# Kernel tuning notes

Hardware: AMD Instinct MI355X
Metric: run time of the kernel (lower is better)

The kernel has to match this reference:

```python
import jax, jax.numpy as jnp
import numpy as np

GAMMA = 0.96875  # RetNet decay, 1 - 2**-5


def setup_inputs() -> dict:
    key = jax.random.key(0)
    kq, kk, kv = jax.random.split(key, 3)
    B, T, D = 8, 4096, 64
    q = jax.random.normal(kq, (B, T, D), dtype=jnp.float32)
    k = jax.random.normal(kk, (B, T, D), dtype=jnp.float32)
    v = jax.random.normal(kv, (B, T, D), dtype=jnp.float32)
    return {"q": q, "k": k, "v": v}


def reference(q, k, v):
    # Parallel retention: out = (QK^T * D_gamma / sqrt(d)) V,
    # D_gamma[i,j] = gamma^(i-j) for i>=j else 0.
    B, T, D = q.shape
    dtype = q.dtype
    idx = jnp.arange(T)
    diff = idx[:, None] - idx[None, :]           # [T,T]
    gamma = jnp.asarray(GAMMA, dtype)
    decay = jnp.where(
        diff >= 0,
        gamma ** jnp.maximum(diff, 0).astype(dtype),
        jnp.zeros((), dtype),
    )                                            # [T,T] causal decay mask
    qk = jnp.einsum('btd,bsd->bts', q, k)        # [B,T,T]
    scale = jnp.asarray(np.sqrt(D), dtype)
    attn = qk * decay[None, :, :] / scale        # [B,T,T]
    out = jnp.einsum('bts,bsd->btd', attn, v)    # [B,T,D]
    return out
```

## Files before the change

kernel.cpp:

```cpp
#include <hip/hip_runtime.h>


using bf16x8 = __attribute__((ext_vector_type(8))) short;
using bf16x4 = __attribute__((ext_vector_type(4))) short;
using f32x4  = __attribute__((ext_vector_type(4))) float;

#define T_SEQ  4096
#define DHEAD  64
#define BM     64
#define BN     64
#define LDSS   72
#define NBACK  3

__device__ __forceinline__ short f2bf(float f) {
  union { float fv; unsigned u; } un; un.fv = f;
  unsigned r = un.u + 0x7FFFu + ((un.u >> 16) & 1u);
  return (short)(r >> 16);
}

__global__ __launch_bounds__(256, 3)
void retention_fwd(const float* __restrict__ qg,
                   const float* __restrict__ kg,
                   const float* __restrict__ vg,
                   float* __restrict__ outg) {
  constexpr float L2G   = -0.04580368961312478f;
  constexpr float GAMMA = 0.96875f;
  constexpr float GI16  = 1.6619242819629204f;
  constexpr float SCALE = 0.125f;

  __shared__ short lds_q [BM * LDSS];
  __shared__ short lds_k [BN * LDSS];
  __shared__ short lds_vt[DHEAD * LDSS];
  __shared__ short lds_p [4 * 16 * LDSS];

  const int tid  = threadIdx.x;
  const int lane = tid & 63;
  const int w    = tid >> 6;
  const int qt   = blockIdx.x & 63;
  const int b    = blockIdx.x >> 6;
  const int iq0  = qt * BM;
  const long base = (long)b * T_SEQ * DHEAD;

  const int ntiles = (qt < NBACK ? qt : NBACK) + 1;

  float4 kreg[4], vreg[4];
  const float4* kbase4 = reinterpret_cast<const float4*>(kg + base);
  const float4* vbase4 = reinterpret_cast<const float4*>(vg + base);

  auto load_kv = [&](int jk0) {
    const float4* ksrc = kbase4 + jk0 * (DHEAD / 4);
    const float4* vsrc = vbase4 + jk0 * (DHEAD / 4);
#pragma unroll
    for (int rep = 0; rep < 4; ++rep) {
      kreg[rep] = ksrc[tid + rep * 256];
      vreg[rep] = vsrc[tid + rep * 256];
    }
  };

  auto stage_kv = [&]() {
#pragma unroll
    for (int rep = 0; rep < 4; ++rep) {
      int idx = tid + rep * 256;
      int row = idx >> 4;
      int c4  = idx & 15;
      bf16x4 s4;
      s4[0] = f2bf(kreg[rep].x); s4[1] = f2bf(kreg[rep].y);
      s4[2] = f2bf(kreg[rep].z); s4[3] = f2bf(kreg[rep].w);
      *reinterpret_cast<bf16x4*>(&lds_k[row * LDSS + c4 * 4]) = s4;
      lds_vt[(c4 * 4 + 0) * LDSS + row] = f2bf(vreg[rep].x);
      lds_vt[(c4 * 4 + 1) * LDSS + row] = f2bf(vreg[rep].y);
      lds_vt[(c4 * 4 + 2) * LDSS + row] = f2bf(vreg[rep].z);
      lds_vt[(c4 * 4 + 3) * LDSS + row] = f2bf(vreg[rep].w);
    }
  };

  {
    const float4* qsrc = reinterpret_cast<const float4*>(qg + base + (long)iq0 * DHEAD);
    float4 qreg[4];
#pragma unroll
    for (int rep = 0; rep < 4; ++rep) qreg[rep] = qsrc[tid + rep * 256];
    load_kv(iq0);
#pragma unroll
    for (int rep = 0; rep < 4; ++rep) {
      int idx = tid + rep * 256;
      int row = idx >> 4;
      int c4  = idx & 15;
      bf16x4 s4;
      s4[0] = f2bf(qreg[rep].x); s4[1] = f2bf(qreg[rep].y);
      s4[2] = f2bf(qreg[rep].z); s4[3] = f2bf(qreg[rep].w);
      *reinterpret_cast<bf16x4*>(&lds_q[row * LDSS + c4 * 4]) = s4;
    }
    stage_kv();
  }
  __syncthreads();

  const int koff = (lane >> 4) * 8;
  const int l15  = lane & 15;
  bf16x8 qf0, qf1;
  {
    int row = w * 16 + l15;
    qf0 = *reinterpret_cast<const bf16x8*>(&lds_q[row * LDSS + koff]);
    qf1 = *reinterpret_cast<const bf16x8*>(&lds_q[row * LDSS + 32 + koff]);
  }

  f32x4 oacc[4];
#pragma unroll
  for (int dt = 0; dt < 4; ++dt) { oacc[dt][0]=0.f; oacc[dt][1]=0.f; oacc[dt][2]=0.f; oacc[dt][3]=0.f; }

  for (int t = 0; t < ntiles; ++t) {
    const int delta = t * BN;
    const bool pf = (t + 1 < ntiles);
    if (pf) load_kv(iq0 - (t + 1) * BN);

    bf16x8 kf[4][2], vf[4][2];
#pragma unroll
    for (int nt = 0; nt < 4; ++nt) {
      int frow = (nt * 16 + l15) * LDSS + koff;
      kf[nt][0] = *reinterpret_cast<const bf16x8*>(&lds_k[frow]);
      kf[nt][1] = *reinterpret_cast<const bf16x8*>(&lds_k[frow + 32]);
      vf[nt][0] = *reinterpret_cast<const bf16x8*>(&lds_vt[frow]);
      vf[nt][1] = *reinterpret_cast<const bf16x8*>(&lds_vt[frow + 32]);
    }
    asm volatile("s_waitcnt lgkmcnt(0)" ::: "memory");
    __syncthreads();

    const int mi = (lane >> 4) * 4;
    const int ebase0 = delta + w * 16 + mi - l15;
    float gq = exp2f((float)ebase0 * L2G) * SCALE;
#pragma unroll
    for (int nt = 0; nt < 4; ++nt) {
      f32x4 s; s[0]=0.f; s[1]=0.f; s[2]=0.f; s[3]=0.f;
      s = __builtin_amdgcn_mfma_f32_16x16x32_bf16(qf0, kf[nt][0], s, 0, 0, 0);
      s = __builtin_amdgcn_mfma_f32_16x16x32_bf16(qf1, kf[nt][1], s, 0, 0, 0);
      const int ebase = ebase0 - nt * 16;
      float g = gq;
#pragma unroll
      for (int r = 0; r < 4; ++r) {
        float sc = ((ebase + r) >= 0) ? g : 0.0f;
        lds_p[(w * 16 + mi + r) * LDSS + nt * 16 + l15] = f2bf(s[r] * sc);
        g *= GAMMA;
      }
      gq *= GI16;
    }
    asm volatile("s_waitcnt lgkmcnt(0)" ::: "memory");

    {
      int prow = (w * 16 + l15) * LDSS + koff;
      bf16x8 pf0 = *reinterpret_cast<const bf16x8*>(&lds_p[prow]);
      bf16x8 pf1 = *reinterpret_cast<const bf16x8*>(&lds_p[prow + 32]);
      __builtin_amdgcn_s_setprio(1);
#pragma unroll
      for (int dt = 0; dt < 4; ++dt) {
        oacc[dt] = __builtin_amdgcn_mfma_f32_16x16x32_bf16(pf0, vf[dt][0], oacc[dt], 0, 0, 0);
        oacc[dt] = __builtin_amdgcn_mfma_f32_16x16x32_bf16(pf1, vf[dt][1], oacc[dt], 0, 0, 0);
      }
      __builtin_amdgcn_s_setprio(0);
    }

    if (pf) stage_kv();
    __syncthreads();
  }

#pragma unroll
  for (int dt = 0; dt < 4; ++dt) {
#pragma unroll
    for (int r = 0; r < 4; ++r) {
      int i = iq0 + w * 16 + (lane >> 4) * 4 + r;
      int d = dt * 16 + l15;
      outg[base + (long)i * DHEAD + d] = oacc[dt][r];
    }
  }
}

extern "C" void kernel_launch(void* const* d_in, const int* in_sizes, int n_in,
                              void* d_out, int out_size, void* d_ws, size_t ws_size,
                              hipStream_t stream) {
  const float* q = (const float*)d_in[0];
  const float* k = (const float*)d_in[1];
  const float* v = (const float*)d_in[2];
  float* out = (float*)d_out;
  int total_rows = in_sizes[0] / DHEAD;
  int nblocks = total_rows / BM;
  retention_fwd<<<dim3(nblocks), dim3(256), 0, stream>>>(q, k, v, out);
}
```

Baseline: 84.61 us.

## Split key tiles across two wave groups per block and reduce partial outputs

Doubles the block to 512 threads. The two halves of four waves each process alternating key tiles for the same query tile, each using its own K/V LDS buffers, and their partial output accumulators are summed through LDS at the end. The aim is to halve the serial tile loop per block (at most 4 tiles become 2 rounds) and raise wave-level parallelism. The cost is a larger LDS footprint (~63KB), which likely limits how many blocks fit per CU, plus an extra reduction step and barriers. K/V fragments are now loaded from LDS inside the compute loop instead of being held in registers beforehand.

```diff
diff --git a/kernel.cpp b/kernel.cpp
--- a/kernel.cpp
+++ b/kernel.cpp
@@ -18,7 +18,7 @@
   return (short)(r >> 16);
 }
 
-__global__ __launch_bounds__(256, 3)
+__global__ __launch_bounds__(512, 4)
 void retention_fwd(const float* __restrict__ qg,
                    const float* __restrict__ kg,
                    const float* __restrict__ vg,
@@ -28,20 +28,29 @@
   constexpr float GI16  = 1.6619242819629204f;
   constexpr float SCALE = 0.125f;
 
-  __shared__ short lds_q [BM * LDSS];
-  __shared__ short lds_k [BN * LDSS];
-  __shared__ short lds_vt[DHEAD * LDSS];
-  __shared__ short lds_p [4 * 16 * LDSS];
+  __shared__ __align__(16) char smem[64512];
+  short* lds_q  = (short*)(smem);
+  short* lds_kb = (short*)(smem + 9216);
+  short* lds_vb = (short*)(smem + 27648);
+  short* lds_p  = (short*)(smem + 46080);
+  float* lds_red= (float*)(smem + 46080);
 
   const int tid  = threadIdx.x;
   const int lane = tid & 63;
   const int w    = tid >> 6;
+  const int mw   = w & 3;
+  const int hw   = w >> 2;
+  const int tid2 = tid & 255;
   const int qt   = blockIdx.x & 63;
   const int b    = blockIdx.x >> 6;
   const int iq0  = qt * BM;
   const long base = (long)b * T_SEQ * DHEAD;
 
-  const int ntiles = (qt < NBACK ? qt : NBACK) + 1;
+  const int ntiles  = (qt < NBACK ? qt : NBACK) + 1;
+  const int nrounds = (ntiles + 1) >> 1;
+
+  short* lds_k  = lds_kb + hw * (BN * LDSS);
+  short* lds_vt = lds_vb + hw * (BN * LDSS);
 
   float4 kreg[4], vreg[4];
   const float4* kbase4 = reinterpret_cast<const float4*>(kg + base);
@@ -52,15 +61,15 @@
     const float4* vsrc = vbase4 + jk0 * (DHEAD / 4);
 #pragma unroll
     for (int rep = 0; rep < 4; ++rep) {
-      kreg[rep] = ksrc[tid + rep * 256];
-      vreg[rep] = vsrc[tid + rep * 256];
+      kreg[rep] = ksrc[tid2 + rep * 256];
+      vreg[rep] = vsrc[tid2 + rep * 256];
     }
   };
 
   auto stage_kv = [&]() {
 #pragma unroll
     for (int rep = 0; rep < 4; ++rep) {
-      int idx = tid + rep * 256;
+      int idx = tid2 + rep * 256;
       int row = idx >> 4;
       int c4  = idx & 15;
       bf16x4 s4;
@@ -75,14 +84,16 @@
   };
 
   {
+    const int t0 = hw;
+    const bool v0 = (t0 < ntiles);
     const float4* qsrc = reinterpret_cast<const float4*>(qg + base + (long)iq0 * DHEAD);
-    float4 qreg[4];
-#pragma unroll
-    for (int rep = 0; rep < 4; ++rep) qreg[rep] = qsrc[tid + rep * 256];
-    load_kv(iq0);
-#pragma unroll
-    for (int rep = 0; rep < 4; ++rep) {
-      int idx = tid + rep * 256;
+    float4 qreg[2];
+#pragma unroll
+    for (int rep = 0; rep < 2; ++rep) qreg[rep] = qsrc[tid + rep * 512];
+    if (v0) load_kv(iq0 - t0 * BN);
+#pragma unroll
+    for (int rep = 0; rep < 2; ++rep) {
+      int idx = tid + rep * 512;
       int row = idx >> 4;
       int c4  = idx & 15;
       bf16x4 s4;
@@ -90,7 +101,7 @@
       s4[2] = f2bf(qreg[rep].z); s4[3] = f2bf(qreg[rep].w);
       *reinterpret_cast<bf16x4*>(&lds_q[row * LDSS + c4 * 4]) = s4;
     }
-    stage_kv();
+    if (v0) stage_kv();
   }
   __syncthreads();
 
@@ -98,7 +109,7 @@
   const int l15  = lane & 15;
   bf16x8 qf0, qf1;
   {
-    int row = w * 16 + l15;
+    int row = mw * 16 + l15;
     qf0 = *reinterpret_cast<const bf16x8*>(&lds_q[row * LDSS + koff]);
     qf1 = *reinterpret_cast<const bf16x8*>(&lds_q[row * LDSS + 32 + koff]);
   }
@@ -107,67 +118,85 @@
 #pragma unroll
   for (int dt = 0; dt < 4; ++dt) { oacc[dt][0]=0.f; oacc[dt][1]=0.f; oacc[dt][2]=0.f; oacc[dt][3]=0.f; }
 
-  for (int t = 0; t < ntiles; ++t) {
-    const int delta = t * BN;
-    const bool pf = (t + 1 < ntiles);
-    if (pf) load_kv(iq0 - (t + 1) * BN);
-
-    bf16x8 kf[4][2], vf[4][2];
-#pragma unroll
-    for (int nt = 0; nt < 4; ++nt) {
-      int frow = (nt * 16 + l15) * LDSS + koff;
-      kf[nt][0] = *reinterpret_cast<const bf16x8*>(&lds_k[frow]);
-      kf[nt][1] = *reinterpret_cast<const bf16x8*>(&lds_k[frow + 32]);
-      vf[nt][0] = *reinterpret_cast<const bf16x8*>(&lds_vt[frow]);
-      vf[nt][1] = *reinterpret_cast<const bf16x8*>(&lds_vt[frow + 32]);
-    }
-    asm volatile("s_waitcnt lgkmcnt(0)" ::: "memory");
-    __syncthreads();
-
-    const int mi = (lane >> 4) * 4;
-    const int ebase0 = delta + w * 16 + mi - l15;
-    float gq = exp2f((float)ebase0 * L2G) * SCALE;
-#pragma unroll
-    for (int nt = 0; nt < 4; ++nt) {
-      f32x4 s; s[0]=0.f; s[1]=0.f; s[2]=0.f; s[3]=0.f;
-      s = __builtin_amdgcn_mfma_f32_16x16x32_bf16(qf0, kf[nt][0], s, 0, 0, 0);
-      s = __builtin_amdgcn_mfma_f32_16x16x32_bf16(qf1, kf[nt][1], s, 0, 0, 0);
-      const int ebase = ebase0 - nt * 16;
-      float g = gq;
-#pragma unroll
-      for (int r = 0; r < 4; ++r) {
-        float sc = ((ebase + r) >= 0) ? g : 0.0f;
-        lds_p[(w * 16 + mi + r) * LDSS + nt * 16 + l15] = f2bf(s[r] * sc);
-        g *= GAMMA;
-      }
-      gq *= GI16;
-    }
-    asm volatile("s_waitcnt lgkmcnt(0)" ::: "memory");
-
-    {
+  for (int r = 0; r < nrounds; ++r) {
+    const int t     = 2 * r + hw;
+    const bool valid = (t < ntiles);
+    const int tn    = t + 2;
+    const bool pf   = (tn < ntiles);
+    if (pf) load_kv(iq0 - tn * BN);
+
+    if (valid) {
+      const int delta = t * BN;
+      const int mi = (lane >> 4) * 4;
+      const int ebase0 = delta + mw * 16 + mi - l15;
+      float gq = exp2f((float)ebase0 * L2G) * SCALE;
+#pragma unroll
+      for (int nt = 0; nt < 4; ++nt) {
+        int krow = (nt * 16 + l15) * LDSS + koff;
+        bf16x8 kf0 = *reinterpret_cast<const bf16x8*>(&lds_k[krow]);
+        bf16x8 kf1 = *reinterpret_cast<const bf16x8*>(&lds_k[krow + 32]);
+        f32x4 s; s[0]=0.f; s[1]=0.f; s[2]=0.f; s[3]=0.f;
+        s = __builtin_amdgcn_mfma_f32_16x16x32_bf16(qf0, kf0, s, 0, 0, 0);
+        s = __builtin_amdgcn_mfma_f32_16x16x32_bf16(qf1, kf1, s, 0, 0, 0);
+        const int ebase = ebase0 - nt * 16;
+        float g = gq;
+#pragma unroll
+        for (int rr = 0; rr < 4; ++rr) {
+          float sc = ((ebase + rr) >= 0) ? g : 0.0f;
+          lds_p[(w * 16 + mi + rr) * LDSS + nt * 16 + l15] = f2bf(s[rr] * sc);
+          g *= GAMMA;
+        }
+        gq *= GI16;
+      }
+      asm volatile("s_waitcnt lgkmcnt(0)" ::: "memory");
+
       int prow = (w * 16 + l15) * LDSS + koff;
       bf16x8 pf0 = *reinterpret_cast<const bf16x8*>(&lds_p[prow]);
       bf16x8 pf1 = *reinterpret_cast<const bf16x8*>(&lds_p[prow + 32]);
       __builtin_amdgcn_s_setprio(1);
 #pragma unroll
       for (int dt = 0; dt < 4; ++dt) {
-        oacc[dt] = __builtin_amdgcn_mfma_f32_16x16x32_bf16(pf0, vf[dt][0], oacc[dt], 0, 0, 0);
-        oacc[dt] = __builtin_amdgcn_mfma_f32_16x16x32_bf16(pf1, vf[dt][1], oacc[dt], 0, 0, 0);
+        int vrow = (dt * 16 + l15) * LDSS + koff;
+        bf16x8 vf0 = *reinterpret_cast<const bf16x8*>(&lds_vt[vrow]);
+        bf16x8 vf1 = *reinterpret_cast<const bf16x8*>(&lds_vt[vrow + 32]);
+        oacc[dt] = __builtin_amdgcn_mfma_f32_16x16x32_bf16(pf0, vf0, oacc[dt], 0, 0, 0);
+        oacc[dt] = __builtin_amdgcn_mfma_f32_16x16x32_bf16(pf1, vf1, oacc[dt], 0, 0, 0);
       }
       __builtin_amdgcn_s_setprio(0);
     }
 
+    __syncthreads();
     if (pf) stage_kv();
+    if (r + 1 < nrounds) __syncthreads();
+  }
+
+  {
+    float* rp = lds_red + (mw * 64 + lane) * 18;
+    if (hw == 1) {
+#pragma unroll
+      for (int dt = 0; dt < 4; ++dt) {
+        *reinterpret_cast<float2*>(rp + dt * 4)     = make_float2(oacc[dt][0], oacc[dt][1]);
+        *reinterpret_cast<float2*>(rp + dt * 4 + 2) = make_float2(oacc[dt][2], oacc[dt][3]);
+      }
+    }
     __syncthreads();
-  }
-
-#pragma unroll
-  for (int dt = 0; dt < 4; ++dt) {
-#pragma unroll
-    for (int r = 0; r < 4; ++r) {
-      int i = iq0 + w * 16 + (lane >> 4) * 4 + r;
-      int d = dt * 16 + l15;
-      outg[base + (long)i * DHEAD + d] = oacc[dt][r];
+    if (hw == 0) {
+#pragma unroll
+      for (int dt = 0; dt < 4; ++dt) {
+        float2 a = *reinterpret_cast<const float2*>(rp + dt * 4);
+        float2 bb= *reinterpret_cast<const float2*>(rp + dt * 4 + 2);
+        oacc[dt][0] += a.x; oacc[dt][1] += a.y;
+        oacc[dt][2] += bb.x; oacc[dt][3] += bb.y;
+      }
+#pragma unroll
+      for (int dt = 0; dt < 4; ++dt) {
+#pragma unroll
+        for (int rr = 0; rr < 4; ++rr) {
+          int i = iq0 + mw * 16 + (lane >> 4) * 4 + rr;
+          int d = dt * 16 + l15;
+          outg[base + (long)i * DHEAD + d] = oacc[dt][rr];
+        }
+      }
     }
   }
 }
@@ -181,5 +210,5 @@
   float* out = (float*)d_out;
   int total_rows = in_sizes[0] / DHEAD;
   int nblocks = total_rows / BM;
-  retention_fwd<<<dim3(nblocks), dim3(256), 0, stream>>>(q, k, v, out);
+  retention_fwd<<<dim3(nblocks), dim3(512), 0, stream>>>(q, k, v, out);
 }
```

Result: no change. 85.62 us (+1.2%).
